# Optimization experiments

Hardware: AMD Instinct MI355X
Metric: run time of the kernel (lower is better)

The kernel has to match this reference:

```python
import jax, jax.numpy as jnp
import numpy as np


def quat_to_rot(q):
    # q: [B, 4] = (x, y, z, w); same math as from_quaternion in the source.
    x, y, z, w = q[:, 0], q[:, 1], q[:, 2], q[:, 3]
    tx, ty, tz = 2.0 * x, 2.0 * y, 2.0 * z
    twx, twy, twz = tx * w, ty * w, tz * w
    txx, txy, txz = tx * x, ty * x, tz * x
    tyy, tyz, tzz = ty * y, tz * y, tz * z
    r = jnp.stack([1.0 - (tyy + tzz), txy - twz, txz + twy,
                   txy + twz, 1.0 - (txx + tzz), tyz - twx,
                   txz - twy, tyz + twx, 1.0 - (txx + tyy)], axis=-1)
    return r.reshape(-1, 3, 3)


def matrix_from_params(transfos):
    B, N = transfos.shape
    R = quat_to_rot(transfos[:, :4])
    if N == 10:
        S = jax.vmap(jnp.diag)(transfos[:, -3:])
    else:
        S = jnp.broadcast_to(jnp.eye(3, dtype=transfos.dtype), (B, 3, 3))
    SR = jnp.matmul(S, R)
    if N == 7:
        t = transfos[:, 4:7][..., None]
    else:
        t = jnp.zeros((B, 3, 1), transfos.dtype)
    return jnp.concatenate([SR, t], axis=2)  # [B, 3, 4]


def spatial_transformer_3d(img, transfos, min_ref_grid, max_ref_grid):
    B, H, W, D, C = img.shape  # ref_size_xyz = (W, H, D) per the source
    theta = matrix_from_params(transfos)  # [B, 3, 4]

    xs = jnp.linspace(min_ref_grid[0], max_ref_grid[0], W)
    ys = jnp.linspace(min_ref_grid[1], max_ref_grid[1], H)
    zs = jnp.linspace(min_ref_grid[2], max_ref_grid[2], D)
    mz, my, mx = jnp.meshgrid(zs, ys, xs, indexing='ij')  # (D, H, W), x fastest
    Nel = D * H * W
    grid = jnp.stack([mx.ravel(), my.ravel(), mz.ravel(),
                      jnp.ones(Nel, dtype=img.dtype)], axis=0)  # (4, Nel)
    pts = jnp.einsum('bij,jn->bin', theta, grid)  # (B, 3, Nel)

    Wf, Hf, Df = float(W), float(H), float(D)
    cx = (Wf - 1.0) / (max_ref_grid[0] - min_ref_grid[0])
    cy = (Hf - 1.0) / (max_ref_grid[1] - min_ref_grid[1])
    cz = (Df - 1.0) / (max_ref_grid[2] - min_ref_grid[2])
    ix = cx * pts[:, 0, :] - cx * min_ref_grid[0]
    iy = cy * pts[:, 1, :] - cy * min_ref_grid[1]
    iz = cz * pts[:, 2, :] - cz * min_ref_grid[2]

    # padding_mode in {'zeros','min'}: validity mask for out-of-grid points
    valid = ((ix >= 0.0) & (ix <= Wf - 1.0) &
             (iy >= 0.0) & (iy <= Hf - 1.0) &
             (iz >= 0.0) & (iz <= Df - 1.0)).astype(img.dtype)[..., None]  # (B, Nel, 1)

    ix0 = jnp.clip(jnp.floor(ix), 0.0, Wf - 1.0)
    iy0 = jnp.clip(jnp.floor(iy), 0.0, Hf - 1.0)
    iz0 = jnp.clip(jnp.floor(iz), 0.0, Df - 1.0)

    imf = img.reshape(B, H * W * D, C)
    acc = jnp.zeros((B, Nel, C), img.dtype)
    for ox in (0.0, 1.0):
        for oy in (0.0, 1.0):
            for oz in (0.0, 1.0):
                gx, gy, gz = ix0 + ox, iy0 + oy, iz0 + oz  # corner coords
                w = (jnp.clip(1.0 - jnp.abs(ix - gx), 0.0, 1.0) *
                     jnp.clip(1.0 - jnp.abs(iy - gy), 0.0, 1.0) *
                     jnp.clip(1.0 - jnp.abs(iz - gz), 0.0, 1.0))
                gxi = jnp.clip(gx, 0.0, Wf - 1.0).astype(jnp.int32)
                gyi = jnp.clip(gy, 0.0, Hf - 1.0).astype(jnp.int32)
                gzi = jnp.clip(gz, 0.0, Df - 1.0).astype(jnp.int32)
                lin = (gyi * W + gxi) * D + gzi  # row-major index into [H, W, D]
                v = jnp.take_along_axis(imf, lin[..., None], axis=1)  # (B, Nel, C)
                acc = acc + w[..., None] * v

    # padding_mode == 'min': fill out-of-grid voxels with the per-volume minimum
    fill = jnp.min(img, axis=(1, 2, 3, 4))[:, None, None]  # (B, 1, 1)
    out = valid * acc + (1.0 - valid) * fill
    # grid was flattened in (z, y, x) order with x fastest -> back to (H, W, D)
    out = out.reshape(B, D, H, W, C).transpose(0, 2, 3, 1, 4)
    return out


def setup_inputs() -> dict:
    key = jax.random.key(0)
    k1, k2 = jax.random.split(key)
    img = jax.random.normal(k1, (4, 160, 160, 160, 1), dtype=jnp.float32)
    transfos = jax.random.normal(k2, (4, 7), dtype=jnp.float32)
    return {"img": img, "transfos": transfos}


def reference(img, transfos):
    min_ref_grid = (-1.0, -1.0, -1.0)
    max_ref_grid = (1.0, 1.0, 1.0)
    return spatial_transformer_3d(img, transfos, min_ref_grid, max_ref_grid)
```

## Files before the change

kernel.cpp:

```cpp
#include <hip/hip_runtime.h>

#define HH 160
#define WW 160
#define DD 160
#define BB 4
#define NPB (HH * WW * DD / 4)
#define K1B 256

typedef float vfloat4 __attribute__((ext_vector_type(4)));

__device__ __forceinline__ unsigned mapf(float f) {
    unsigned b = __float_as_uint(f);
    return (b & 0x80000000u) ? ~b : (b | 0x80000000u);
}
__device__ __forceinline__ float unmapf(unsigned k) {
    unsigned b = (k & 0x80000000u) ? (k ^ 0x80000000u) : ~k;
    return __uint_as_float(b);
}


__global__ __launch_bounds__(256) void min_cst_kernel(const float4* __restrict__ img4,
                                                      const float* __restrict__ transfos,
                                                      unsigned* __restrict__ minkey,
                                                      double* __restrict__ cst) {
    const int b = blockIdx.y;
    const size_t base = (size_t)b * NPB;
    const int t0 = blockIdx.x * 256 + threadIdx.x;
    const int S = K1B * 256;

    float m = 3.4e38f;
    #pragma unroll
    for (int r = 0; r < 4; r++) {
        const int i0 = t0 + 4 * r * S;
        float4 v0 = img4[base + i0];
        float4 v1 = img4[base + i0 + S];
        float4 v2 = img4[base + i0 + 2 * S];
        float4 v3 = make_float4(3.4e38f, 3.4e38f, 3.4e38f, 3.4e38f);
        if (i0 + 3 * S < NPB) v3 = img4[base + i0 + 3 * S];
        m = fminf(m, fminf(fminf(v0.x, v0.y), fminf(v0.z, v0.w)));
        m = fminf(m, fminf(fminf(v1.x, v1.y), fminf(v1.z, v1.w)));
        m = fminf(m, fminf(fminf(v2.x, v2.y), fminf(v2.z, v2.w)));
        m = fminf(m, fminf(fminf(v3.x, v3.y), fminf(v3.z, v3.w)));
    }

    #pragma unroll
    for (int o = 32; o >= 1; o >>= 1) m = fminf(m, __shfl_down(m, o));
    __shared__ float s[4];
    const int lane = threadIdx.x & 63, wid = threadIdx.x >> 6;
    if (lane == 0) s[wid] = m;
    __syncthreads();
    if (threadIdx.x == 0) {
        m = fminf(fminf(s[0], s[1]), fminf(s[2], s[3]));
        atomicMin(&minkey[b * 64], mapf(m));
    }

    if (blockIdx.x == 0 && blockIdx.y == 0 && threadIdx.x < BB) {
        const int bb = threadIdx.x;
        const float* q = transfos + bb * 7;
        double x = q[0], y = q[1], z = q[2], w = q[3];
        double tx = 2.0 * x, ty = 2.0 * y, tz = 2.0 * z;
        double twx = tx * w, twy = ty * w, twz = tz * w;
        double txx = tx * x, txy = ty * x, txz = tz * x;
        double tyy = ty * y, tyz = tz * y, tzz = tz * z;
        double R[3][3] = {
            {1.0 - (tyy + tzz), txy - twz,         txz + twy},
            {txy + twz,         1.0 - (txx + tzz), tyz - twx},
            {txz - twy,         tyz + twx,         1.0 - (txx + tyy)}
        };
        double t[3] = {(double)q[4], (double)q[5], (double)q[6]};
        for (int r = 0; r < 3; r++) {
            cst[bb * 12 + r * 4 + 0] = R[r][0];
            cst[bb * 12 + r * 4 + 1] = R[r][1];
            cst[bb * 12 + r * 4 + 2] = R[r][2];
            cst[bb * 12 + r * 4 + 3] = 79.5 * (t[r] - R[r][0] - R[r][1] - R[r][2] + 1.0);
        }
    }
}

__global__ __launch_bounds__(256) void st3d_kernel(const float* __restrict__ img,
                                                   const double* __restrict__ cst,
                                                   const unsigned* __restrict__ minkey,
                                                   float* __restrict__ out) {
    const int b = blockIdx.z;
    const int y = blockIdx.y;
    const float fill = unmapf(minkey[b * 64]);

    const int t = blockIdx.x * 256 + threadIdx.x;
    const int x = t / 40;
    const int zq = (t - 40 * x) * 4;

    const double* c = cst + b * 12;
    const double c2 = c[2], c6 = c[6], c10 = c[10];
    const double dx = (double)x, dy = (double)y, dz = (double)zq;
    double jx = fma(c[0], dx, fma(c[1], dy, fma(c2, dz, c[3])));
    double jy = fma(c[4], dx, fma(c[5], dy, fma(c6, dz, c[7])));
    double jz = fma(c[8], dx, fma(c[9], dy, fma(c10, dz, c[11])));

    const float* base = img + (size_t)b * (HH * WW * DD);

    bool vld[4];
    float fx[4], fy[4], fz[4];
    const float* pp[4][4];
    int zz0[4], zz1[4];
    #pragma unroll
    for (int k = 0; k < 4; k++) {
        vld[k] = (jx >= 0.0) && (jx <= 159.0) && (jy >= 0.0) && (jy <= 159.0) &&
                 (jz >= 0.0) && (jz <= 159.0);
        double flx = floor(jx), fly = floor(jy), flz = floor(jz);
        int x0 = (int)flx, y0 = (int)fly, z0 = (int)flz;
        fx[k] = (float)(jx - flx); fy[k] = (float)(jy - fly); fz[k] = (float)(jz - flz);
        int x1 = min(x0 + 1, 159), y1 = min(y0 + 1, 159), z1 = min(z0 + 1, 159);
        pp[k][0] = base + ((size_t)y0 * WW + x0) * DD;
        pp[k][1] = base + ((size_t)y1 * WW + x0) * DD;
        pp[k][2] = base + ((size_t)y0 * WW + x1) * DD;
        pp[k][3] = base + ((size_t)y1 * WW + x1) * DD;
        zz0[k] = z0; zz1[k] = z1;
        jx += c2; jy += c6; jz += c10;
    }

    float v[4][8];
    #pragma unroll
    for (int k = 0; k < 4; k++) {
        if (vld[k]) {
            v[k][0] = pp[k][0][zz0[k]]; v[k][1] = pp[k][0][zz1[k]];
            v[k][2] = pp[k][1][zz0[k]]; v[k][3] = pp[k][1][zz1[k]];
            v[k][4] = pp[k][2][zz0[k]]; v[k][5] = pp[k][2][zz1[k]];
            v[k][6] = pp[k][3][zz0[k]]; v[k][7] = pp[k][3][zz1[k]];
        }
    }

    vfloat4 r;
    #pragma unroll
    for (int k = 0; k < 4; k++) {
        float wx0 = 1.0f - fx[k], wx1 = fx[k];
        float wy0 = 1.0f - fy[k], wy1 = fy[k];
        float wz0 = 1.0f - fz[k], wz1 = fz[k];
        float a;
        a  = ((wx0 * wy0) * wz0) * v[k][0];
        a += ((wx0 * wy0) * wz1) * v[k][1];
        a += ((wx0 * wy1) * wz0) * v[k][2];
        a += ((wx0 * wy1) * wz1) * v[k][3];
        a += ((wx1 * wy0) * wz0) * v[k][4];
        a += ((wx1 * wy0) * wz1) * v[k][5];
        a += ((wx1 * wy1) * wz0) * v[k][6];
        a += ((wx1 * wy1) * wz1) * v[k][7];
        r[k] = vld[k] ? a : fill;
    }

    vfloat4* outp = (vfloat4*)(out + (size_t)(b * HH + y) * (WW * DD) + x * DD + zq);
    *outp = r;
}

extern "C" void kernel_launch(void* const* d_in, const int* in_sizes, int n_in,
                              void* d_out, int out_size, void* d_ws, size_t ws_size,
                              hipStream_t stream) {
    const float* img = (const float*)d_in[0];
    const float* transfos = (const float*)d_in[1];
    float* out = (float*)d_out;
    unsigned* minkey = (unsigned*)d_ws;
    double* cst = (double*)((char*)d_ws + 4096);

    (void)hipMemsetAsync(minkey, 0xFF, 1024, stream);
    min_cst_kernel<<<dim3(K1B, BB), 256, 0, stream>>>((const float4*)img, transfos,
                                                      minkey, cst);
    st3d_kernel<<<dim3(25, 160, BB), 256, 0, stream>>>(img, cst, minkey, out);
}
```

Measured before the change: 136.0 us.

## Loop each thread over a chunk of y rows and skip rows outside the volume analytically

```diff
diff --git a/kernel.cpp b/kernel.cpp
--- a/kernel.cpp
+++ b/kernel.cpp
@@ -6,6 +6,7 @@
 #define BB 4
 #define NPB (HH * WW * DD / 4)
 #define K1B 256
+#define YC 20
 
 typedef float vfloat4 __attribute__((ext_vector_type(4)));
 
@@ -82,7 +83,7 @@
                                                    const unsigned* __restrict__ minkey,
                                                    float* __restrict__ out) {
     const int b = blockIdx.z;
-    const int y = blockIdx.y;
+    const int ybase = blockIdx.y * YC;
     const float fill = unmapf(minkey[b * 64]);
 
     const int t = blockIdx.x * 256 + threadIdx.x;
@@ -90,65 +91,95 @@
     const int zq = (t - 40 * x) * 4;
 
     const double* c = cst + b * 12;
-    const double c2 = c[2], c6 = c[6], c10 = c[10];
-    const double dx = (double)x, dy = (double)y, dz = (double)zq;
-    double jx = fma(c[0], dx, fma(c[1], dy, fma(c2, dz, c[3])));
-    double jy = fma(c[4], dx, fma(c[5], dy, fma(c6, dz, c[7])));
-    double jz = fma(c[8], dx, fma(c[9], dy, fma(c10, dz, c[11])));
+    const double dx = (double)x, dzq = (double)zq;
+
+    double wlo = -1e300, whi = 1e300;
+    bool empty = false;
+    #pragma unroll
+    for (int r = 0; r < 3; r++) {
+        const double Cc = c[4 * r + 1];
+        const double Cz = c[4 * r + 2];
+        const double A0 = fma(c[4 * r], dx, fma(Cz, dzq, c[4 * r + 3]));
+        const double A3 = A0 + 3.0 * Cz;
+        const double Amin = fmin(A0, A3), Amax = fmax(A0, A3);
+        if (Cc == 0.0) {
+            empty |= (Amax < 0.0) || (Amin > 159.0);
+        } else {
+            const double t0 = (0.0 - Amax) / Cc;
+            const double t1 = (159.0 - Amin) / Cc;
+            wlo = fmax(wlo, fmin(t0, t1));
+            whi = fmin(whi, fmax(t0, t1));
+        }
+    }
+    int ywlo = 1, ywhi = 0;
+    if (!empty && whi >= wlo) {
+        const double a = fmax(wlo - 1.0, 0.0);
+        const double bnd = fmin(whi + 1.0, 159.0);
+        if (bnd >= a) { ywlo = (int)a; ywhi = (int)bnd; }
+    }
 
     const float* base = img + (size_t)b * (HH * WW * DD);
+    const double c2 = c[2], c6 = c[6], c10 = c[10];
+    float* outp = out + (size_t)(b * HH + ybase) * (WW * DD) + x * DD + zq;
 
-    bool vld[4];
-    float fx[4], fy[4], fz[4];
-    const float* pp[4][4];
-    int zz0[4], zz1[4];
-    #pragma unroll
-    for (int k = 0; k < 4; k++) {
-        vld[k] = (jx >= 0.0) && (jx <= 159.0) && (jy >= 0.0) && (jy <= 159.0) &&
-                 (jz >= 0.0) && (jz <= 159.0);
-        double flx = floor(jx), fly = floor(jy), flz = floor(jz);
-        int x0 = (int)flx, y0 = (int)fly, z0 = (int)flz;
-        fx[k] = (float)(jx - flx); fy[k] = (float)(jy - fly); fz[k] = (float)(jz - flz);
-        int x1 = min(x0 + 1, 159), y1 = min(y0 + 1, 159), z1 = min(z0 + 1, 159);
-        pp[k][0] = base + ((size_t)y0 * WW + x0) * DD;
-        pp[k][1] = base + ((size_t)y1 * WW + x0) * DD;
-        pp[k][2] = base + ((size_t)y0 * WW + x1) * DD;
-        pp[k][3] = base + ((size_t)y1 * WW + x1) * DD;
-        zz0[k] = z0; zz1[k] = z1;
-        jx += c2; jy += c6; jz += c10;
+    for (int y = ybase; y < ybase + YC; y++, outp += WW * DD) {
+        vfloat4 r = {fill, fill, fill, fill};
+        if (y >= ywlo && y <= ywhi) {
+            const double dy = (double)y;
+            double jx = fma(c[0], dx, fma(c[1], dy, fma(c2, dzq, c[3])));
+            double jy = fma(c[4], dx, fma(c[5], dy, fma(c6, dzq, c[7])));
+            double jz = fma(c[8], dx, fma(c[9], dy, fma(c10, dzq, c[11])));
+
+            bool vld[4];
+            float fx[4], fy[4], fz[4];
+            const float* pp[4][4];
+            int zz0[4], zz1[4];
+            #pragma unroll
+            for (int k = 0; k < 4; k++) {
+                vld[k] = (jx >= 0.0) && (jx <= 159.0) && (jy >= 0.0) && (jy <= 159.0) &&
+                         (jz >= 0.0) && (jz <= 159.0);
+                double flx = floor(jx), fly = floor(jy), flz = floor(jz);
+                int x0 = (int)flx, y0 = (int)fly, z0 = (int)flz;
+                fx[k] = (float)(jx - flx); fy[k] = (float)(jy - fly); fz[k] = (float)(jz - flz);
+                int x1 = min(x0 + 1, 159), y1 = min(y0 + 1, 159), z1 = min(z0 + 1, 159);
+                pp[k][0] = base + ((size_t)y0 * WW + x0) * DD;
+                pp[k][1] = base + ((size_t)y1 * WW + x0) * DD;
+                pp[k][2] = base + ((size_t)y0 * WW + x1) * DD;
+                pp[k][3] = base + ((size_t)y1 * WW + x1) * DD;
+                zz0[k] = z0; zz1[k] = z1;
+                jx += c2; jy += c6; jz += c10;
+            }
+
+            float v[4][8];
+            #pragma unroll
+            for (int k = 0; k < 4; k++) {
+                if (vld[k]) {
+                    v[k][0] = pp[k][0][zz0[k]]; v[k][1] = pp[k][0][zz1[k]];
+                    v[k][2] = pp[k][1][zz0[k]]; v[k][3] = pp[k][1][zz1[k]];
+                    v[k][4] = pp[k][2][zz0[k]]; v[k][5] = pp[k][2][zz1[k]];
+                    v[k][6] = pp[k][3][zz0[k]]; v[k][7] = pp[k][3][zz1[k]];
+                }
+            }
+
+            #pragma unroll
+            for (int k = 0; k < 4; k++) {
+                float wx0 = 1.0f - fx[k], wx1 = fx[k];
+                float wy0 = 1.0f - fy[k], wy1 = fy[k];
+                float wz0 = 1.0f - fz[k], wz1 = fz[k];
+                float a;
+                a  = ((wx0 * wy0) * wz0) * v[k][0];
+                a += ((wx0 * wy0) * wz1) * v[k][1];
+                a += ((wx0 * wy1) * wz0) * v[k][2];
+                a += ((wx0 * wy1) * wz1) * v[k][3];
+                a += ((wx1 * wy0) * wz0) * v[k][4];
+                a += ((wx1 * wy0) * wz1) * v[k][5];
+                a += ((wx1 * wy1) * wz0) * v[k][6];
+                a += ((wx1 * wy1) * wz1) * v[k][7];
+                if (vld[k]) r[k] = a;
+            }
+        }
+        *(vfloat4*)outp = r;
     }
-
-    float v[4][8];
-    #pragma unroll
-    for (int k = 0; k < 4; k++) {
-        if (vld[k]) {
-            v[k][0] = pp[k][0][zz0[k]]; v[k][1] = pp[k][0][zz1[k]];
-            v[k][2] = pp[k][1][zz0[k]]; v[k][3] = pp[k][1][zz1[k]];
-            v[k][4] = pp[k][2][zz0[k]]; v[k][5] = pp[k][2][zz1[k]];
-            v[k][6] = pp[k][3][zz0[k]]; v[k][7] = pp[k][3][zz1[k]];
-        }
-    }
-
-    vfloat4 r;
-    #pragma unroll
-    for (int k = 0; k < 4; k++) {
-        float wx0 = 1.0f - fx[k], wx1 = fx[k];
-        float wy0 = 1.0f - fy[k], wy1 = fy[k];
-        float wz0 = 1.0f - fz[k], wz1 = fz[k];
-        float a;
-        a  = ((wx0 * wy0) * wz0) * v[k][0];
-        a += ((wx0 * wy0) * wz1) * v[k][1];
-        a += ((wx0 * wy1) * wz0) * v[k][2];
-        a += ((wx0 * wy1) * wz1) * v[k][3];
-        a += ((wx1 * wy0) * wz0) * v[k][4];
-        a += ((wx1 * wy0) * wz1) * v[k][5];
-        a += ((wx1 * wy1) * wz0) * v[k][6];
-        a += ((wx1 * wy1) * wz1) * v[k][7];
-        r[k] = vld[k] ? a : fill;
-    }
-
-    vfloat4* outp = (vfloat4*)(out + (size_t)(b * HH + y) * (WW * DD) + x * DD + zq);
-    *outp = r;
 }
 
 extern "C" void kernel_launch(void* const* d_in, const int* in_sizes, int n_in,
@@ -163,5 +194,5 @@
     (void)hipMemsetAsync(minkey, 0xFF, 1024, stream);
     min_cst_kernel<<<dim3(K1B, BB), 256, 0, stream>>>((const float4*)img, transfos,
                                                       minkey, cst);
-    st3d_kernel<<<dim3(25, 160, BB), 256, 0, stream>>>(img, cst, minkey, out);
+    st3d_kernel<<<dim3(25, 8, BB), 256, 0, stream>>>(img, cst, minkey, out);
 }
```

Result: slower. 199.1 us (+46.4%).
